# Kernel tuning notes

Measured on AMD Instinct MI355X. Metric: run time of the kernel, lower is better.

## Reference

```python
import jax, jax.numpy as jnp
import numpy as np

B, C, H, W = 16, 512, 32, 32
G = min(C // 4, 32)  # group-norm groups = 32
EPS = 1e-6


def setup_inputs() -> dict:
    key = jax.random.key(0)
    ks = jax.random.split(key, 9)
    s = 1.0 / np.sqrt(C)
    return {
        "x": jax.random.normal(ks[0], (B, C, H, W), dtype=jnp.float32),
        "gn_gamma": jnp.ones((C,), jnp.float32),
        "gn_beta": jnp.zeros((C,), jnp.float32),
        "W0": jax.random.normal(ks[1], (C, C), jnp.float32) * s,
        "b0": jnp.zeros((C,), jnp.float32),
        "W1": jax.random.normal(ks[2], (C, C), jnp.float32) * s,
        "b1": jnp.zeros((C,), jnp.float32),
        "W2": jax.random.normal(ks[3], (C, C), jnp.float32) * s,
        "b2": jnp.zeros((C,), jnp.float32),
        "W3": jax.random.normal(ks[4], (C, C), jnp.float32) * s,
        "b3": jnp.zeros((C,), jnp.float32),
    }


def _group_norm(x, gamma, beta):
    b, c, h, w = x.shape
    xg = x.reshape(b, G, c // G, h, w)
    mu = jnp.mean(xg, axis=(2, 3, 4), keepdims=True)
    var = jnp.var(xg, axis=(2, 3, 4), keepdims=True)
    xn = ((xg - mu) * jax.lax.rsqrt(var + EPS)).reshape(b, c, h, w)
    return xn * gamma[None, :, None, None] + beta[None, :, None, None]


def _nin(x, Wm, bv):
    # 1x1 conv via channel contraction: bchw,cd->bdhw
    return jnp.einsum('bchw,cd->bdhw', x, Wm) + bv[None, :, None, None]


def reference(x, gn_gamma, gn_beta, W0, b0, W1, b1, W2, b2, W3, b3):
    b, c, h, w = x.shape
    hn = _group_norm(x, gn_gamma, gn_beta)
    q = _nin(hn, W0, b0)
    k = _nin(hn, W1, b1)
    v = _nin(hn, W2, b2)
    # attention scores over all spatial positions: [b, h, w, i, j]
    scores = jnp.einsum('bchw,bcij->bhwij', q, k) * (c ** -0.5)
    attn = jax.nn.softmax(scores.reshape(b, h, w, h * w), axis=-1).reshape(b, h, w, h, w)
    o = jnp.einsum('bhwij,bcij->bchw', attn, v)
    o = _nin(o, W3, b3)
    return x + o  # skip_rescale=False
```

## Files before the change

kernel.cpp:

```cpp
#include <hip/hip_runtime.h>
#include <stdint.h>

typedef __bf16 bf16_t;
typedef _Float16 f16_t;
typedef bf16_t bf16x8 __attribute__((ext_vector_type(8)));
typedef bf16_t bf16x4 __attribute__((ext_vector_type(4)));
typedef f16_t  f16x8  __attribute__((ext_vector_type(8)));
typedef f16_t  f16x4  __attribute__((ext_vector_type(4)));
typedef float floatx4 __attribute__((ext_vector_type(4)));

static constexpr int NB  = 16;
static constexpr int NC  = 512;
static constexpr int NHW = 1024;
static constexpr int NG  = 32;
static constexpr int CPG = 16;

#define SCALE 0.044194173824159216f
#define LOG2E 1.4426950408889634f

__global__ __launch_bounds__(256) void gn_stats_k(const float* __restrict__ x,
                                                  float* __restrict__ stats) {
  int bg = blockIdx.x;
  const float* xp = x + (size_t)bg * CPG * NHW;
  float s = 0.f, ss = 0.f;
  for (int i = threadIdx.x * 4; i < CPG * NHW; i += 256 * 4) {
    float4 v = *(const float4*)&xp[i];
    s += v.x + v.y + v.z + v.w;
    ss += v.x * v.x + v.y * v.y + v.z * v.z + v.w * v.w;
  }
#pragma unroll
  for (int off = 1; off < 64; off <<= 1) {
    s  += __shfl_xor(s,  off, 64);
    ss += __shfl_xor(ss, off, 64);
  }
  __shared__ float red[2][4];
  int wv = threadIdx.x >> 6;
  if ((threadIdx.x & 63) == 0) { red[0][wv] = s; red[1][wv] = ss; }
  __syncthreads();
  if (threadIdx.x == 0) {
    float st  = red[0][0] + red[0][1] + red[0][2] + red[0][3];
    float sst = red[1][0] + red[1][1] + red[1][2] + red[1][3];
    float mean = st * (1.f / 16384.f);
    float var  = sst * (1.f / 16384.f) - mean * mean;
    stats[bg * 2]     = mean;
    stats[bg * 2 + 1] = rsqrtf(var + 1e-6f);
  }
}

__global__ __launch_bounds__(256) void gn_apply_k(const float* __restrict__ x,
                                                  const float* __restrict__ gamma,
                                                  const float* __restrict__ beta,
                                                  const float* __restrict__ stats,
                                                  bf16_t* __restrict__ hnT,
                                                  bf16_t* __restrict__ hnN) {
  int bi = blockIdx.z;
  int c0 = blockIdx.y * 32;
  int n0 = blockIdx.x * 32;
  __shared__ float tile[32][33];
  int tn = threadIdx.x & 31;
  int tr = threadIdx.x >> 5;
  const float* xb = x + (size_t)bi * NC * NHW;
#pragma unroll
  for (int r = 0; r < 4; r++) {
    int c = c0 + tr + r * 8;
    int g = c >> 4;
    float mean = stats[(bi * NG + g) * 2];
    float rstd = stats[(bi * NG + g) * 2 + 1];
    float ga = gamma[c], be = beta[c];
    float v = xb[(size_t)c * NHW + n0 + tn];
    tile[tr + r * 8][tn] = (v - mean) * rstd * ga + be;
  }
  __syncthreads();
  int rl = threadIdx.x >> 3, ch = (threadIdx.x & 7) * 4;
  bf16_t* hb = hnT + (size_t)bi * NHW * NC;
  bf16x4 pk;
#pragma unroll
  for (int i = 0; i < 4; i++) pk[i] = (bf16_t)tile[ch + i][rl];
  *(bf16x4*)&hb[(size_t)(n0 + rl) * NC + c0 + ch] = pk;
  bf16_t* hc = hnN + (size_t)bi * NC * NHW;
  bf16x4 pk2;
#pragma unroll
  for (int i = 0; i < 4; i++) pk2[i] = (bf16_t)tile[rl][ch + i];
  *(bf16x4*)&hc[(size_t)(c0 + rl) * NHW + n0 + ch] = pk2;
}

__global__ __launch_bounds__(256) void wtrans_k(const float* __restrict__ W0,
                                                const float* __restrict__ W1,
                                                const float* __restrict__ W2,
                                                const float* __restrict__ W3,
                                                bf16_t* __restrict__ Wt) {
  int w = blockIdx.z;
  const float* W = (w == 0) ? W0 : (w == 1) ? W1 : (w == 2) ? W2 : W3;
  bf16_t* o = Wt + (size_t)w * NC * NC;
  int d0 = blockIdx.x * 32, c0 = blockIdx.y * 32;
  if (w == 2) {
    int cl = threadIdx.x >> 3, dc = (threadIdx.x & 7) * 4;
    float4 v = *(const float4*)&W[(size_t)(c0 + cl) * NC + d0 + dc];
    bf16x4 pk;
    pk[0] = (bf16_t)v.x; pk[1] = (bf16_t)v.y; pk[2] = (bf16_t)v.z; pk[3] = (bf16_t)v.w;
    *(bf16x4*)&o[(size_t)(c0 + cl) * NC + d0 + dc] = pk;
    return;
  }
  __shared__ float tile[32][33];
  int tdx = threadIdx.x & 31, tr = threadIdx.x >> 5;
#pragma unroll
  for (int r = 0; r < 4; r++)
    tile[tr + r * 8][tdx] = W[(size_t)(c0 + tr + r * 8) * NC + d0 + tdx];
  __syncthreads();
  int dl = threadIdx.x >> 3, cc = (threadIdx.x & 7) * 4;
  bf16x4 pk;
#pragma unroll
  for (int i = 0; i < 4; i++) pk[i] = (bf16_t)tile[cc + i][dl];
  *(bf16x4*)&o[(size_t)(d0 + dl) * NC + c0 + cc] = pk;
}

__global__ __launch_bounds__(256) void bias_k(const float* __restrict__ b2,
                                              const float* __restrict__ W3,
                                              const float* __restrict__ b3,
                                              float* __restrict__ bb) {
  int e = blockIdx.x * 256 + threadIdx.x;
  float s = b3[e];
  for (int d = 0; d < NC; d++) s += b2[d] * W3[(size_t)d * NC + e];
  bb[e] = s;
}

__device__ __forceinline__ void glds16(const bf16_t* g, bf16_t* lds) {
  __builtin_amdgcn_global_load_lds(
      (const __attribute__((address_space(1))) unsigned int*)g,
      (__attribute__((address_space(3))) unsigned int*)lds, 16, 0, 0);
}

__device__ __forceinline__ floatx4 mfma_bf16(bf16x8 a, bf16x8 b, floatx4 c) {
  return __builtin_amdgcn_mfma_f32_16x16x32_bf16(a, b, c, 0, 0, 0);
}

template<int KDIM, bool SWAP>
__device__ __forceinline__ void gemm_core(const bf16_t* __restrict__ A,
                                          const bf16_t* __restrict__ B,
                                          int m0, int n0,
                                          floatx4 (&acc)[4][4]) {
  __shared__ bf16_t As[128 * 64];
  __shared__ bf16_t Bs[128 * 64];
  const int tid = threadIdx.x, lane = tid & 63, wv = tid >> 6;
  const int l16 = lane & 15, quad = lane >> 4;
  const int wm = wv & 1, wn = wv >> 1;
  const int x7 = l16 & 7;

  const int srow = lane >> 3;
  const int schunk = (lane & 7) ^ srow;
  const bf16_t* aptr = A + (size_t)(m0 + wv * 32 + srow) * KDIM + schunk * 8;
  const bf16_t* bptr = B + (size_t)(n0 + wv * 32 + srow) * KDIM + schunk * 8;
  bf16_t* as_ = &As[(wv * 32) * 64];
  bf16_t* bs_ = &Bs[(wv * 32) * 64];

  for (int k0 = 0; k0 < KDIM; k0 += 64) {
    __syncthreads();
#pragma unroll
    for (int i = 0; i < 4; i++) {
      glds16(aptr + (size_t)(8 * i) * KDIM, as_ + (8 * i) * 64);
      glds16(bptr + (size_t)(8 * i) * KDIM, bs_ + (8 * i) * 64);
    }
    aptr += 64; bptr += 64;
    __syncthreads();
    bf16x8 af[2][4], bfv[2][4];
#pragma unroll
    for (int h = 0; h < 2; h++)
#pragma unroll
      for (int i = 0; i < 4; i++) {
        int q = h * 4 + quad;
        af[h][i]  = *(const bf16x8*)&As[(wm * 64 + i * 16 + l16) * 64 + ((q ^ x7) * 8)];
        bfv[h][i] = *(const bf16x8*)&Bs[(wn * 64 + i * 16 + l16) * 64 + ((q ^ x7) * 8)];
      }
#pragma unroll
    for (int h = 0; h < 2; h++)
#pragma unroll
      for (int i = 0; i < 4; i++)
#pragma unroll
        for (int j = 0; j < 4; j++)
          acc[i][j] = SWAP ? mfma_bf16(bfv[h][j], af[h][i], acc[i][j])
                           : mfma_bf16(af[h][i], bfv[h][j], acc[i][j]);
  }
}

#define ACC_INIT(acc)                                   \
  floatx4 acc[4][4];                                    \
  _Pragma("unroll") for (int i = 0; i < 4; i++)         \
  _Pragma("unroll") for (int j = 0; j < 4; j++)         \
    acc[i][j] = (floatx4){0.f, 0.f, 0.f, 0.f};

__global__ __launch_bounds__(256) void w23_k(const bf16_t* __restrict__ Wt3,
                                             const bf16_t* __restrict__ W2b,
                                             bf16_t* __restrict__ W23t) {
  int n0 = blockIdx.x * 128, m0 = blockIdx.y * 128;
  ACC_INIT(acc);
  gemm_core<NC, false>(Wt3, W2b, m0, n0, acc);
  const int lane = threadIdx.x & 63, wv = threadIdx.x >> 6;
  const int l16 = lane & 15, quad = lane >> 4, wm = wv & 1, wn = wv >> 1;
#pragma unroll
  for (int i = 0; i < 4; i++)
#pragma unroll
    for (int j = 0; j < 4; j++) {
      int row = m0 + wm * 64 + i * 16 + quad * 4;
      int col = n0 + wn * 64 + j * 16 + l16;
#pragma unroll
      for (int r = 0; r < 4; r++)
        W23t[(size_t)(row + r) * NC + col] = (bf16_t)acc[i][j][r];
    }
}

__global__ __launch_bounds__(256) void gemm_qk_k(const bf16_t* __restrict__ hnT,
                                                 const bf16_t* __restrict__ Wt,
                                                 const float* __restrict__ b0,
                                                 const float* __restrict__ b1,
                                                 bf16_t* __restrict__ Qt,
                                                 bf16_t* __restrict__ Kt) {
  int bz = blockIdx.z, bi = bz & 15, wsel = bz >> 4;
  int n0 = blockIdx.x * 128, m0 = blockIdx.y * 128;
  const bf16_t* A = hnT + (size_t)bi * NHW * NC;
  const bf16_t* B = Wt + (size_t)wsel * NC * NC;
  ACC_INIT(acc);
  gemm_core<NC, true>(A, B, m0, n0, acc);

  const int lane = threadIdx.x & 63, wv = threadIdx.x >> 6;
  const int l16 = lane & 15, quad = lane >> 4, wm = wv & 1, wn = wv >> 1;
  const float* bias = wsel ? b1 : b0;
  const float sc = wsel ? 1.f : SCALE;
  bf16_t* out = (wsel ? Kt : Qt) + (size_t)bi * NHW * NC;
#pragma unroll
  for (int i = 0; i < 4; i++) {
    int m = m0 + wm * 64 + i * 16 + l16;
#pragma unroll
    for (int j = 0; j < 4; j++) {
      int db = n0 + wn * 64 + j * 16 + quad * 4;
      float4 bv = *(const float4*)&bias[db];
      bf16x4 pk;
      pk[0] = (bf16_t)((acc[i][j][0] + bv.x) * sc);
      pk[1] = (bf16_t)((acc[i][j][1] + bv.y) * sc);
      pk[2] = (bf16_t)((acc[i][j][2] + bv.z) * sc);
      pk[3] = (bf16_t)((acc[i][j][3] + bv.w) * sc);
      *(bf16x4*)&out[(size_t)m * NC + db] = pk;
    }
  }
}

__global__ __launch_bounds__(256) void gemm_s_k(const bf16_t* __restrict__ Qt,
                                                const bf16_t* __restrict__ Kt,
                                                f16_t* __restrict__ S) {
  int bi = blockIdx.z;
  int n0 = blockIdx.x * 128, m0 = blockIdx.y * 128;
  const bf16_t* A = Qt + (size_t)bi * NHW * NC;
  const bf16_t* B = Kt + (size_t)bi * NHW * NC;
  ACC_INIT(acc);
  gemm_core<NC, true>(A, B, m0, n0, acc);

  const int lane = threadIdx.x & 63, wv = threadIdx.x >> 6;
  const int l16 = lane & 15, quad = lane >> 4, wm = wv & 1, wn = wv >> 1;
  f16_t* out = S + (size_t)bi * NHW * NHW;
#pragma unroll
  for (int i = 0; i < 4; i++) {
    int m = m0 + wm * 64 + i * 16 + l16;
#pragma unroll
    for (int j = 0; j < 4; j++) {
      int nb = n0 + wn * 64 + j * 16 + quad * 4;
      f16x4 pk;
#pragma unroll
      for (int r = 0; r < 4; r++) pk[r] = (f16_t)(acc[i][j][r]);
      *(f16x4*)&out[(size_t)m * NHW + nb] = pk;
    }
  }
}

__global__ __launch_bounds__(256) void softmax_k(const f16_t* __restrict__ S,
                                                 bf16_t* __restrict__ P) {
  int row = blockIdx.x * 4 + (threadIdx.x >> 6);
  int lane = threadIdx.x & 63;
  const f16_t* sp = S + (size_t)row * NHW + lane * 16;
  f16x8 a = *(const f16x8*)sp;
  f16x8 b = *(const f16x8*)(sp + 8);
  float v[16];
#pragma unroll
  for (int k = 0; k < 8; k++) { v[k] = (float)a[k]; v[8 + k] = (float)b[k]; }
  float mx = v[0];
#pragma unroll
  for (int k = 1; k < 16; k++) mx = fmaxf(mx, v[k]);
#pragma unroll
  for (int off = 1; off < 64; off <<= 1) mx = fmaxf(mx, __shfl_xor(mx, off, 64));
  float e[16], s = 0.f;
#pragma unroll
  for (int k = 0; k < 16; k++) { e[k] = exp2f((v[k] - mx) * LOG2E); s += e[k]; }
#pragma unroll
  for (int off = 1; off < 64; off <<= 1) s += __shfl_xor(s, off, 64);
  float inv = 1.f / s;
  bf16x8 o0, o1;
#pragma unroll
  for (int k = 0; k < 8; k++) { o0[k] = (bf16_t)(e[k] * inv); o1[k] = (bf16_t)(e[8 + k] * inv); }
  bf16_t* pp = P + (size_t)row * NHW + lane * 16;
  *(bf16x8*)pp = o0;
  *(bf16x8*)(pp + 8) = o1;
}

__global__ __launch_bounds__(256) void gemm_t_k(const bf16_t* __restrict__ P,
                                                const bf16_t* __restrict__ hnN,
                                                bf16_t* __restrict__ T) {
  int bi = blockIdx.z;
  int n0 = blockIdx.x * 128, m0 = blockIdx.y * 128;
  const bf16_t* A = P + (size_t)bi * NHW * NHW;
  const bf16_t* B = hnN + (size_t)bi * NC * NHW;
  ACC_INIT(acc);
  gemm_core<NHW, true>(A, B, m0, n0, acc);

  const int lane = threadIdx.x & 63, wv = threadIdx.x >> 6;
  const int l16 = lane & 15, quad = lane >> 4, wm = wv & 1, wn = wv >> 1;
  bf16_t* out = T + (size_t)bi * NHW * NC;
#pragma unroll
  for (int i = 0; i < 4; i++) {
    int m = m0 + wm * 64 + i * 16 + l16;
#pragma unroll
    for (int j = 0; j < 4; j++) {
      int cb = n0 + wn * 64 + j * 16 + quad * 4;
      bf16x4 pk;
#pragma unroll
      for (int r = 0; r < 4; r++) pk[r] = (bf16_t)(acc[i][j][r]);
      *(bf16x4*)&out[(size_t)m * NC + cb] = pk;
    }
  }
}

__global__ __launch_bounds__(256) void gemm_out_k(const bf16_t* __restrict__ T,
                                                  const bf16_t* __restrict__ W23t,
                                                  const float* __restrict__ bb,
                                                  const float* __restrict__ x,
                                                  float* __restrict__ outp) {
  int bi = blockIdx.z;
  int n0 = blockIdx.x * 128, m0 = blockIdx.y * 128;
  const bf16_t* A = T + (size_t)bi * NHW * NC;
  ACC_INIT(acc);
  gemm_core<NC, false>(A, W23t, m0, n0, acc);

  const int lane = threadIdx.x & 63, wv = threadIdx.x >> 6;
  const int l16 = lane & 15, quad = lane >> 4, wm = wv & 1, wn = wv >> 1;
  const float* xb = x + (size_t)bi * NC * NHW;
  float* ob = outp + (size_t)bi * NC * NHW;
#pragma unroll
  for (int i = 0; i < 4; i++)
#pragma unroll
    for (int j = 0; j < 4; j++) {
      int row = m0 + wm * 64 + i * 16 + quad * 4;
      int col = n0 + wn * 64 + j * 16 + l16;
      float bv = bb[col];
      size_t base = (size_t)col * NHW + row;
      float4 xv = *(const float4*)&xb[base];
      float4 pk;
      pk.x = acc[i][j][0] + bv + xv.x;
      pk.y = acc[i][j][1] + bv + xv.y;
      pk.z = acc[i][j][2] + bv + xv.z;
      pk.w = acc[i][j][3] + bv + xv.w;
      *(float4*)&ob[base] = pk;
    }
}

extern "C" void kernel_launch(void* const* d_in, const int* in_sizes, int n_in,
                              void* d_out, int out_size, void* d_ws, size_t ws_size,
                              hipStream_t stream) {
  (void)in_sizes; (void)n_in; (void)out_size; (void)ws_size;
  const float* x     = (const float*)d_in[0];
  const float* gamma = (const float*)d_in[1];
  const float* beta  = (const float*)d_in[2];
  const float* W0    = (const float*)d_in[3];
  const float* b0    = (const float*)d_in[4];
  const float* W1    = (const float*)d_in[5];
  const float* b1    = (const float*)d_in[6];
  const float* W2    = (const float*)d_in[7];
  const float* b2    = (const float*)d_in[8];
  const float* W3    = (const float*)d_in[9];
  const float* b3    = (const float*)d_in[10];
  float* outp = (float*)d_out;

  char* ws = (char*)d_ws;
  const size_t PLANE = (size_t)NB * NHW * NC * sizeof(bf16_t);
  float* stats = (float*)ws;
  size_t off = 4096;
  bf16_t* hnT = (bf16_t*)(ws + off); off += PLANE;
  bf16_t* hnN = (bf16_t*)(ws + off); off += PLANE;
  bf16_t* Qt  = (bf16_t*)(ws + off); off += PLANE;
  bf16_t* Kt  = (bf16_t*)(ws + off); off += PLANE;
  bf16_t* Wt  = (bf16_t*)(ws + off); off += 4 * (size_t)NC * NC * sizeof(bf16_t);
  bf16_t* W23t = (bf16_t*)(ws + off); off += (size_t)NC * NC * sizeof(bf16_t);
  float*  bb  = (float*)(ws + off);  off += 4096;
  f16_t*  S   = (f16_t*)(ws + off);  off += (size_t)NB * NHW * NHW * sizeof(f16_t);
  bf16_t* P   = (bf16_t*)S;
  bf16_t* T   = hnT;

  gn_stats_k<<<NB * NG, 256, 0, stream>>>(x, stats);
  gn_apply_k<<<dim3(32, 16, NB), 256, 0, stream>>>(x, gamma, beta, stats, hnT, hnN);
  wtrans_k<<<dim3(16, 16, 4), 256, 0, stream>>>(W0, W1, W2, W3, Wt);
  w23_k<<<dim3(4, 4, 1), 256, 0, stream>>>(Wt + 3 * (size_t)NC * NC, Wt + 2 * (size_t)NC * NC, W23t);
  bias_k<<<dim3(2), 256, 0, stream>>>(b2, W3, b3, bb);
  gemm_qk_k<<<dim3(4, 8, 32), 256, 0, stream>>>(hnT, Wt, b0, b1, Qt, Kt);
  gemm_s_k<<<dim3(8, 8, NB), 256, 0, stream>>>(Qt, Kt, S);
  softmax_k<<<dim3(NB * NHW / 4), 256, 0, stream>>>(S, P);
  gemm_t_k<<<dim3(4, 8, NB), 256, 0, stream>>>(P, hnN, T);
  gemm_out_k<<<dim3(4, 8, NB), 256, 0, stream>>>(T, W23t, bb, x, outp);
}
```

Measured before the change: 268.0 us.

## Fold Q and K projections into a single W0·W1ᵀ bilinear form

Scores are now computed as hn·(W0 W1ᵀ)·hnᵀ. A precomputed 512x512 matrix M turns the two Q/K projection GEMMs into a single G = hn·M GEMM, and the S GEMM uses hn directly as the key operand. Bias terms that vary along the key index are folded into a per-column vector w = hn·(W1 b0) that softmax adds. Terms constant across a softmax row are dropped because they cancel. This halves the projection GEMM work and its memory traffic, and merges the small weight-prep kernels. In exchange the rounding changes, since M is stored in bf16.

```diff
diff --git a/kernel.cpp b/kernel.cpp
--- a/kernel.cpp
+++ b/kernel.cpp
@@ -84,16 +84,21 @@
   *(bf16x4*)&hc[(size_t)(c0 + rl) * NHW + n0 + ch] = pk2;
 }
 
-__global__ __launch_bounds__(256) void wtrans_k(const float* __restrict__ W0,
+__global__ __launch_bounds__(256) void wprep1_k(const float* __restrict__ W0,
                                                 const float* __restrict__ W1,
                                                 const float* __restrict__ W2,
                                                 const float* __restrict__ W3,
-                                                bf16_t* __restrict__ Wt) {
-  int w = blockIdx.z;
-  const float* W = (w == 0) ? W0 : (w == 1) ? W1 : (w == 2) ? W2 : W3;
-  bf16_t* o = Wt + (size_t)w * NC * NC;
-  int d0 = blockIdx.x * 32, c0 = blockIdx.y * 32;
-  if (w == 2) {
+                                                const float* __restrict__ b0,
+                                                const float* __restrict__ b2,
+                                                const float* __restrict__ b3,
+                                                bf16_t* __restrict__ Wt,
+                                                float* __restrict__ u,
+                                                float* __restrict__ bb) {
+  int z = blockIdx.z;
+  if (z < 3) {
+    const float* W = (z == 0) ? W0 : (z == 1) ? W1 : W2;
+    bf16_t* o = Wt + (size_t)z * NC * NC;
+    int d0 = blockIdx.x * 32, c0 = blockIdx.y * 32;
     int cl = threadIdx.x >> 3, dc = (threadIdx.x & 7) * 4;
     float4 v = *(const float4*)&W[(size_t)(c0 + cl) * NC + d0 + dc];
     bf16x4 pk;
@@ -101,27 +106,64 @@
     *(bf16x4*)&o[(size_t)(c0 + cl) * NC + d0 + dc] = pk;
     return;
   }
-  __shared__ float tile[32][33];
-  int tdx = threadIdx.x & 31, tr = threadIdx.x >> 5;
-#pragma unroll
-  for (int r = 0; r < 4; r++)
-    tile[tr + r * 8][tdx] = W[(size_t)(c0 + tr + r * 8) * NC + d0 + tdx];
-  __syncthreads();
-  int dl = threadIdx.x >> 3, cc = (threadIdx.x & 7) * 4;
-  bf16x4 pk;
-#pragma unroll
-  for (int i = 0; i < 4; i++) pk[i] = (bf16_t)tile[cc + i][dl];
-  *(bf16x4*)&o[(size_t)(d0 + dl) * NC + c0 + cc] = pk;
-}
-
-__global__ __launch_bounds__(256) void bias_k(const float* __restrict__ b2,
-                                              const float* __restrict__ W3,
-                                              const float* __restrict__ b3,
-                                              float* __restrict__ bb) {
-  int e = blockIdx.x * 256 + threadIdx.x;
-  float s = b3[e];
-  for (int d = 0; d < NC; d++) s += b2[d] * W3[(size_t)d * NC + e];
-  bb[e] = s;
+  if (z == 3) {
+    bf16_t* o = Wt + (size_t)3 * NC * NC;
+    int d0 = blockIdx.x * 32, c0 = blockIdx.y * 32;
+    __shared__ float tile[32][33];
+    int tdx = threadIdx.x & 31, tr = threadIdx.x >> 5;
+#pragma unroll
+    for (int r = 0; r < 4; r++)
+      tile[tr + r * 8][tdx] = W3[(size_t)(c0 + tr + r * 8) * NC + d0 + tdx];
+    __syncthreads();
+    int dl = threadIdx.x >> 3, cc = (threadIdx.x & 7) * 4;
+    bf16x4 pk;
+#pragma unroll
+    for (int i = 0; i < 4; i++) pk[i] = (bf16_t)tile[cc + i][dl];
+    *(bf16x4*)&o[(size_t)(d0 + dl) * NC + c0 + cc] = pk;
+    return;
+  }
+  int bx = blockIdx.x, by = blockIdx.y;
+  if (by < 8) {
+    int cblock = by * 16 + bx;
+    int wv = threadIdx.x >> 6, lane = threadIdx.x & 63;
+    int c = cblock * 4 + wv;
+    const float* wr = W1 + (size_t)c * NC + lane * 8;
+    float s = 0.f;
+#pragma unroll
+    for (int k = 0; k < 8; k++) s += wr[k] * b0[lane * 8 + k];
+#pragma unroll
+    for (int off = 1; off < 64; off <<= 1) s += __shfl_xor(s, off, 64);
+    if (lane == 0) u[c] = SCALE * s;
+    return;
+  }
+  if (by == 8 && bx < 8) {
+    int e0 = bx * 64;
+    int el = threadIdx.x & 63, sl = threadIdx.x >> 6;
+    float s = 0.f;
+    for (int d = sl * 128; d < sl * 128 + 128; d++)
+      s += b2[d] * W3[(size_t)d * NC + e0 + el];
+    __shared__ float red[4][64];
+    red[sl][el] = s;
+    __syncthreads();
+    if (threadIdx.x < 64)
+      bb[e0 + threadIdx.x] = red[0][threadIdx.x] + red[1][threadIdx.x] +
+                             red[2][threadIdx.x] + red[3][threadIdx.x] + b3[e0 + threadIdx.x];
+  }
+}
+
+__global__ __launch_bounds__(256) void w_k(const bf16_t* __restrict__ hnT,
+                                           const float* __restrict__ u,
+                                           float* __restrict__ w) {
+  int row = blockIdx.x * 4 + (threadIdx.x >> 6);
+  int lane = threadIdx.x & 63;
+  bf16x8 h = *(const bf16x8*)&hnT[(size_t)row * NC + lane * 8];
+  const float* up = u + lane * 8;
+  float s = 0.f;
+#pragma unroll
+  for (int k = 0; k < 8; k++) s += (float)h[k] * up[k];
+#pragma unroll
+  for (int off = 1; off < 64; off <<= 1) s += __shfl_xor(s, off, 64);
+  if (lane == 0) w[row] = s;
 }
 
 __device__ __forceinline__ void glds16(const bf16_t* g, bf16_t* lds) {
@@ -188,12 +230,17 @@
   _Pragma("unroll") for (int j = 0; j < 4; j++)         \
     acc[i][j] = (floatx4){0.f, 0.f, 0.f, 0.f};
 
-__global__ __launch_bounds__(256) void w23_k(const bf16_t* __restrict__ Wt3,
-                                             const bf16_t* __restrict__ W2b,
-                                             bf16_t* __restrict__ W23t) {
+__global__ __launch_bounds__(256) void wprep2_k(const bf16_t* __restrict__ Wt,
+                                                bf16_t* __restrict__ Mt,
+                                                bf16_t* __restrict__ W23t) {
+  int z = blockIdx.z;
+  const bf16_t* A = (z == 0) ? (Wt + (size_t)1 * NC * NC) : (Wt + (size_t)3 * NC * NC);
+  const bf16_t* B = (z == 0) ? (Wt + (size_t)0 * NC * NC) : (Wt + (size_t)2 * NC * NC);
+  bf16_t* out = (z == 0) ? Mt : W23t;
+  const float sc = (z == 0) ? SCALE : 1.f;
   int n0 = blockIdx.x * 128, m0 = blockIdx.y * 128;
   ACC_INIT(acc);
-  gemm_core<NC, false>(Wt3, W2b, m0, n0, acc);
+  gemm_core<NC, false>(A, B, m0, n0, acc);
   const int lane = threadIdx.x & 63, wv = threadIdx.x >> 6;
   const int l16 = lane & 15, quad = lane >> 4, wm = wv & 1, wn = wv >> 1;
 #pragma unroll
@@ -204,52 +251,39 @@
       int col = n0 + wn * 64 + j * 16 + l16;
 #pragma unroll
       for (int r = 0; r < 4; r++)
-        W23t[(size_t)(row + r) * NC + col] = (bf16_t)acc[i][j][r];
-    }
-}
-
-__global__ __launch_bounds__(256) void gemm_qk_k(const bf16_t* __restrict__ hnT,
-                                                 const bf16_t* __restrict__ Wt,
-                                                 const float* __restrict__ b0,
-                                                 const float* __restrict__ b1,
-                                                 bf16_t* __restrict__ Qt,
-                                                 bf16_t* __restrict__ Kt) {
-  int bz = blockIdx.z, bi = bz & 15, wsel = bz >> 4;
+        out[(size_t)(row + r) * NC + col] = (bf16_t)(acc[i][j][r] * sc);
+    }
+}
+
+__global__ __launch_bounds__(256) void gemm_g_k(const bf16_t* __restrict__ hnT,
+                                                const bf16_t* __restrict__ Mt,
+                                                bf16_t* __restrict__ G) {
   int n0 = blockIdx.x * 128, m0 = blockIdx.y * 128;
-  const bf16_t* A = hnT + (size_t)bi * NHW * NC;
-  const bf16_t* B = Wt + (size_t)wsel * NC * NC;
   ACC_INIT(acc);
-  gemm_core<NC, true>(A, B, m0, n0, acc);
-
+  gemm_core<NC, true>(hnT, Mt, m0, n0, acc);
   const int lane = threadIdx.x & 63, wv = threadIdx.x >> 6;
   const int l16 = lane & 15, quad = lane >> 4, wm = wv & 1, wn = wv >> 1;
-  const float* bias = wsel ? b1 : b0;
-  const float sc = wsel ? 1.f : SCALE;
-  bf16_t* out = (wsel ? Kt : Qt) + (size_t)bi * NHW * NC;
 #pragma unroll
   for (int i = 0; i < 4; i++) {
     int m = m0 + wm * 64 + i * 16 + l16;
 #pragma unroll
     for (int j = 0; j < 4; j++) {
-      int db = n0 + wn * 64 + j * 16 + quad * 4;
-      float4 bv = *(const float4*)&bias[db];
+      int eb = n0 + wn * 64 + j * 16 + quad * 4;
       bf16x4 pk;
-      pk[0] = (bf16_t)((acc[i][j][0] + bv.x) * sc);
-      pk[1] = (bf16_t)((acc[i][j][1] + bv.y) * sc);
-      pk[2] = (bf16_t)((acc[i][j][2] + bv.z) * sc);
-      pk[3] = (bf16_t)((acc[i][j][3] + bv.w) * sc);
-      *(bf16x4*)&out[(size_t)m * NC + db] = pk;
-    }
-  }
-}
-
-__global__ __launch_bounds__(256) void gemm_s_k(const bf16_t* __restrict__ Qt,
-                                                const bf16_t* __restrict__ Kt,
+#pragma unroll
+      for (int r = 0; r < 4; r++) pk[r] = (bf16_t)(acc[i][j][r]);
+      *(bf16x4*)&G[(size_t)m * NC + eb] = pk;
+    }
+  }
+}
+
+__global__ __launch_bounds__(256) void gemm_s_k(const bf16_t* __restrict__ G,
+                                                const bf16_t* __restrict__ hnT,
                                                 f16_t* __restrict__ S) {
   int bi = blockIdx.z;
   int n0 = blockIdx.x * 128, m0 = blockIdx.y * 128;
-  const bf16_t* A = Qt + (size_t)bi * NHW * NC;
-  const bf16_t* B = Kt + (size_t)bi * NHW * NC;
+  const bf16_t* A = G + (size_t)bi * NHW * NC;
+  const bf16_t* B = hnT + (size_t)bi * NHW * NC;
   ACC_INIT(acc);
   gemm_core<NC, true>(A, B, m0, n0, acc);
 
@@ -271,15 +305,18 @@
 }
 
 __global__ __launch_bounds__(256) void softmax_k(const f16_t* __restrict__ S,
+                                                 const float* __restrict__ w,
                                                  bf16_t* __restrict__ P) {
   int row = blockIdx.x * 4 + (threadIdx.x >> 6);
   int lane = threadIdx.x & 63;
+  int b = row >> 10;
   const f16_t* sp = S + (size_t)row * NHW + lane * 16;
+  const float* wp = w + b * NHW + lane * 16;
   f16x8 a = *(const f16x8*)sp;
-  f16x8 b = *(const f16x8*)(sp + 8);
+  f16x8 bq = *(const f16x8*)(sp + 8);
   float v[16];
 #pragma unroll
-  for (int k = 0; k < 8; k++) { v[k] = (float)a[k]; v[8 + k] = (float)b[k]; }
+  for (int k = 0; k < 8; k++) { v[k] = (float)a[k] + wp[k]; v[8 + k] = (float)bq[k] + wp[8 + k]; }
   float mx = v[0];
 #pragma unroll
   for (int k = 1; k < 16; k++) mx = fmaxf(mx, v[k]);
@@ -369,7 +406,7 @@
   const float* W0    = (const float*)d_in[3];
   const float* b0    = (const float*)d_in[4];
   const float* W1    = (const float*)d_in[5];
-  const float* b1    = (const float*)d_in[6];
+  const float* b1    = (const float*)d_in[6];  (void)b1;
   const float* W2    = (const float*)d_in[7];
   const float* b2    = (const float*)d_in[8];
   const float* W3    = (const float*)d_in[9];
@@ -382,23 +419,25 @@
   size_t off = 4096;
   bf16_t* hnT = (bf16_t*)(ws + off); off += PLANE;
   bf16_t* hnN = (bf16_t*)(ws + off); off += PLANE;
-  bf16_t* Qt  = (bf16_t*)(ws + off); off += PLANE;
-  bf16_t* Kt  = (bf16_t*)(ws + off); off += PLANE;
+  bf16_t* G   = (bf16_t*)(ws + off); off += PLANE;
   bf16_t* Wt  = (bf16_t*)(ws + off); off += 4 * (size_t)NC * NC * sizeof(bf16_t);
+  bf16_t* Mt   = (bf16_t*)(ws + off); off += (size_t)NC * NC * sizeof(bf16_t);
   bf16_t* W23t = (bf16_t*)(ws + off); off += (size_t)NC * NC * sizeof(bf16_t);
-  float*  bb  = (float*)(ws + off);  off += 4096;
+  float*  u   = (float*)(ws + off);  off += 2048;
+  float*  bb  = (float*)(ws + off);  off += 2048;
+  float*  w   = (float*)(ws + off);  off += (size_t)NB * NHW * sizeof(float);
   f16_t*  S   = (f16_t*)(ws + off);  off += (size_t)NB * NHW * NHW * sizeof(f16_t);
   bf16_t* P   = (bf16_t*)S;
-  bf16_t* T   = hnT;
+  bf16_t* T   = G;
 
   gn_stats_k<<<NB * NG, 256, 0, stream>>>(x, stats);
   gn_apply_k<<<dim3(32, 16, NB), 256, 0, stream>>>(x, gamma, beta, stats, hnT, hnN);
-  wtrans_k<<<dim3(16, 16, 4), 256, 0, stream>>>(W0, W1, W2, W3, Wt);
-  w23_k<<<dim3(4, 4, 1), 256, 0, stream>>>(Wt + 3 * (size_t)NC * NC, Wt + 2 * (size_t)NC * NC, W23t);
-  bias_k<<<dim3(2), 256, 0, stream>>>(b2, W3, b3, bb);
-  gemm_qk_k<<<dim3(4, 8, 32), 256, 0, stream>>>(hnT, Wt, b0, b1, Qt, Kt);
-  gemm_s_k<<<dim3(8, 8, NB), 256, 0, stream>>>(Qt, Kt, S);
-  softmax_k<<<dim3(NB * NHW / 4), 256, 0, stream>>>(S, P);
+  wprep1_k<<<dim3(16, 16, 5), 256, 0, stream>>>(W0, W1, W2, W3, b0, b2, b3, Wt, u, bb);
+  wprep2_k<<<dim3(4, 4, 2), 256, 0, stream>>>(Wt, Mt, W23t);
+  w_k<<<dim3(NB * NHW / 4), 256, 0, stream>>>(hnT, u, w);
+  gemm_g_k<<<dim3(4, 128), 256, 0, stream>>>(hnT, Mt, G);
+  gemm_s_k<<<dim3(8, 8, NB), 256, 0, stream>>>(G, hnT, S);
+  softmax_k<<<dim3(NB * NHW / 4), 256, 0, stream>>>(S, w, P);
   gemm_t_k<<<dim3(4, 8, NB), 256, 0, stream>>>(P, hnN, T);
   gemm_out_k<<<dim3(4, 8, NB), 256, 0, stream>>>(T, W23t, bb, x, outp);
 }
```

Measured after the change: 245.6 us. 1.09x faster.
